# Performance work log

Hardware: AMD Instinct MI355X
Metric: run time of the kernel (lower is better)

Reference implementation:

```python
import jax, jax.numpy as jnp
import numpy as np

N_NODES = 10000
N_EDGES = 16384
D = 128            # node_in_dim == out_dim == edge_attr_dim == hidden_dim


def setup_inputs() -> dict:
    key = jax.random.key(0)
    ks = jax.random.split(key, 9)
    s = 1.0 / np.sqrt(D)
    x = jax.random.normal(ks[0], (N_NODES, D), dtype=jnp.float32)
    edge_index = jax.random.randint(ks[1], (2, N_EDGES), 0, N_NODES, dtype=jnp.int64)
    edge_attr = jax.random.normal(ks[2], (N_EDGES, D), dtype=jnp.float32)
    # edge_net: MLP 128 -> 128 (ReLU) -> 128*128
    w1 = jax.random.normal(ks[3], (D, D), dtype=jnp.float32) * s
    b1 = jnp.zeros((D,), dtype=jnp.float32)
    w2 = jax.random.normal(ks[4], (D, D * D), dtype=jnp.float32) * s
    b2 = jnp.zeros((D * D,), dtype=jnp.float32)
    # NNConv root weight and bias
    root = jax.random.normal(ks[5], (D, D), dtype=jnp.float32) * s
    bias = jnp.zeros((D,), dtype=jnp.float32)
    return {"x": x, "edge_index": edge_index, "edge_attr": edge_attr,
            "w1": w1, "b1": b1, "w2": w2, "b2": b2, "root": root, "bias": bias}


def reference(x, edge_index, edge_attr, w1, b1, w2, b2, root, bias):
    src, dst = edge_index[0], edge_index[1]
    # edge_net -> per-edge weight matrices [E, D, D]
    h = jax.nn.relu(edge_attr @ w1 + b1)
    w_edge = (h @ w2 + b2).reshape(-1, D, D)
    # gather source features, per-edge matvec: [E, D]
    x_j = x[src]
    msg = jnp.einsum('ei,eio->eo', x_j, w_edge)
    # scatter-mean into destination nodes
    seg_sum = jax.ops.segment_sum(msg, dst, num_segments=N_NODES)
    cnt = jax.ops.segment_sum(jnp.ones((msg.shape[0],), msg.dtype), dst,
                              num_segments=N_NODES)
    aggr = seg_sum / jnp.maximum(cnt, 1.0)[:, None]
    # NNConv root transform + bias
    conv_out = aggr + x @ root + bias
    # residual + exact GELU (torch nn.GELU default)
    return x + jax.nn.gelu(conv_out, approximate=False)
```

## Files before the change

### kernel.cpp

```cpp
#include <hip/hip_runtime.h>
#include <math.h>

#define D 128
#define NNODES 10000
#define NEDGES 16384
#define PADR 136
#define MAXDEG 16

typedef short short8 __attribute__((ext_vector_type(8)));
typedef float floatx4 __attribute__((ext_vector_type(4)));
typedef unsigned short ushortx4 __attribute__((ext_vector_type(4)));

__device__ __forceinline__ float bf2f(unsigned short u) {
  union { unsigned u; float f; } v; v.u = ((unsigned)u) << 16; return v.f;
}
__device__ __forceinline__ unsigned short f2bf(float f) {
  union { float f; unsigned u; } v; v.f = f;
  return (unsigned short)((v.u + 0x7FFFu + ((v.u >> 16) & 1u)) >> 16);
}
__device__ __forceinline__ float bflo(unsigned u) {
  union { unsigned u; float f; } v; v.u = u << 16; return v.f;
}
__device__ __forceinline__ float bfhi(unsigned u) {
  union { unsigned u; float f; } v; v.u = u & 0xFFFF0000u; return v.f;
}
__device__ __forceinline__ short8 pack8(float4 a, float4 b) {
  short8 r;
  r[0] = (short)f2bf(a.x); r[1] = (short)f2bf(a.y);
  r[2] = (short)f2bf(a.z); r[3] = (short)f2bf(a.w);
  r[4] = (short)f2bf(b.x); r[5] = (short)f2bf(b.y);
  r[6] = (short)f2bf(b.z); r[7] = (short)f2bf(b.w);
  return r;
}

__global__ __launch_bounds__(256) void k12(
    const float* __restrict__ x, const int* __restrict__ eidx,
    const float* __restrict__ ea,
    const float* __restrict__ w1, const float* __restrict__ b1,
    const float* __restrict__ w2, const float* __restrict__ b2,
    const float* __restrict__ root,
    unsigned short* __restrict__ w2t, unsigned short* __restrict__ rootT,
    unsigned short* __restrict__ hT, unsigned short* __restrict__ xjb,
    int* __restrict__ cnt) {
  __shared__ float L[32][129];
  __shared__ unsigned short w1tL[128 * PADR];
  const int t = threadIdx.x;
  const int bid = blockIdx.x;

  if (bid < 520) {
    if (bid < 40) { const int gid = bid * 256 + t; if (gid < NNODES) cnt[gid] = 0; }
    const float* __restrict__ src;
    unsigned short* dst;
    int o0;
    if (bid < 516) {
      const int k = bid >> 2;
      o0 = (bid & 3) * 32;
      src = (k < D) ? (w2 + (long)k * (D * D)) : b2;
      dst = w2t + (long)k * (D * PADR);
    } else {
      o0 = (bid - 516) * 32; src = root; dst = rootT;
    }
#pragma unroll
    for (int r = 0; r < 16; ++r) {
      int idx = r * 256 + t;
      int i = idx >> 5, oc = idx & 31;
      L[oc][i] = src[i * D + o0 + oc];
    }
    __syncthreads();
#pragma unroll
    for (int r = 0; r < 8; ++r) {
      int p = r * 256 + t;
      int oc = p >> 6, i2 = (p & 63) * 2;
      unsigned v = (unsigned)f2bf(L[oc][i2]) | ((unsigned)f2bf(L[oc][i2 + 1]) << 16);
      *(unsigned*)(dst + ((o0 + oc) * PADR + i2)) = v;
    }
    return;
  }

  const int e0 = (bid - 520) * 64;
#pragma unroll 4
  for (int r = 0; r < 16; ++r) {
    int idx = r * 256 + t, e = idx >> 6, i2 = (idx & 63) * 2;
    const int s = eidx[e0 + e];
    const float2 v = *(const float2*)(x + (long)s * D + i2);
    unsigned p = (unsigned)f2bf(v.x) | ((unsigned)f2bf(v.y) << 16);
    *(unsigned*)(xjb + ((e0 + e) * PADR + i2)) = p;
  }
  for (int c = 0; c < 4; ++c) {
    const int o0c = c * 32;
#pragma unroll
    for (int r = 0; r < 16; ++r) {
      int idx = r * 256 + t;
      int i = idx >> 5, oc = idx & 31;
      L[oc][i] = w1[i * D + o0c + oc];
    }
    __syncthreads();
#pragma unroll
    for (int r = 0; r < 8; ++r) {
      int p = r * 256 + t;
      int oc = p >> 6, i2 = (p & 63) * 2;
      unsigned v = (unsigned)f2bf(L[oc][i2]) | ((unsigned)f2bf(L[oc][i2 + 1]) << 16);
      *(unsigned*)(w1tL + ((o0c + oc) * PADR + i2)) = v;
    }
    __syncthreads();
  }
  const int lane = t & 63, w = t >> 6, lo = lane & 15, hi = lane >> 4;
  short8 af[4];
#pragma unroll
  for (int ks = 0; ks < 4; ++ks) {
    const float* p0 = ea + (long)(e0 + w * 16 + lo) * D + ks * 32 + hi * 8;
    af[ks] = pack8(*(const float4*)p0, *(const float4*)(p0 + 4));
  }
  floatx4 acc[8];
#pragma unroll
  for (int nt = 0; nt < 8; ++nt) acc[nt] = (floatx4){0.f, 0.f, 0.f, 0.f};
#pragma unroll
  for (int ks = 0; ks < 4; ++ks) {
    const int ib = ks * 32 + hi * 8;
#pragma unroll
    for (int nt = 0; nt < 8; ++nt) {
      const short8 bf_ = *(const short8*)&w1tL[(nt * 16 + lo) * PADR + ib];
      acc[nt] = __builtin_amdgcn_mfma_f32_16x16x32_bf16(af[ks], bf_, acc[nt], 0, 0, 0);
    }
  }
#pragma unroll
  for (int nt = 0; nt < 8; ++nt) {
    const int ko = nt * 16 + lo;
    const float b1v = b1[ko];
    float v0 = fmaxf(acc[nt][0] + b1v, 0.f);
    float v1 = fmaxf(acc[nt][1] + b1v, 0.f);
    float v2 = fmaxf(acc[nt][2] + b1v, 0.f);
    float v3 = fmaxf(acc[nt][3] + b1v, 0.f);
    uint2 pk;
    pk.x = (unsigned)f2bf(v0) | ((unsigned)f2bf(v1) << 16);
    pk.y = (unsigned)f2bf(v2) | ((unsigned)f2bf(v3) << 16);
    *(uint2*)(hT + (ko * NEDGES + e0 + w * 16 + hi * 4)) = pk;
  }
  if (t < 64) hT[128 * NEDGES + e0 + t] = 0x3F80;
}

__global__ __launch_bounds__(256, 3) void k3_msg(
    const unsigned short* __restrict__ w2t,
    const unsigned short* __restrict__ xjb,
    const unsigned short* __restrict__ hT,
    const int* __restrict__ eidx, int* __restrict__ cnt,
    int* __restrict__ elist,
    unsigned short* __restrict__ msgout) {
  __shared__ float hLT[65 * 128];
  const int t = threadIdx.x;
  const int b = blockIdx.x;
  const int kh = b & 1;
  const int oq = (b >> 1) & 3;
  const int eg = b >> 3;
  const int e0 = eg * 128;
  const int o0 = oq * 32;
  const int kbase = kh * 64;
  const int kcnt = kh ? 65 : 64;
  const int lane = t & 63, wv = t >> 6;
  const int lo = lane & 15, hi = lane >> 4;
  const int we = (wv >> 1) * 64;
  const int wo = (wv & 1) * 16;

  if ((b & 7) == 0 && t < 128) {
    const int e = e0 + t;
    const int d = eidx[NEDGES + e];
    const int pos = atomicAdd(&cnt[d], 1);
    if (pos < MAXDEG) elist[d * MAXDEG + pos] = e;
  }

  for (int idx = t; idx < kcnt * 64; idx += 256) {
    const int kk = idx >> 6, e2 = (idx & 63) * 2;
    const unsigned u = *(const unsigned*)&hT[(long)(kbase + kk) * NEDGES + e0 + e2];
    const int ebase = kk * 128;
#pragma unroll
    for (int q = 0; q < 2; ++q) {
      const int e = e2 + q;
      hLT[ebase + ((e >> 6) << 6) + ((e & 15) << 2) + ((e >> 4) & 3)] =
          q ? bfhi(u) : bflo(u);
    }
  }

  short8 xf[4][4];
#pragma unroll
  for (int ne = 0; ne < 4; ++ne)
#pragma unroll
    for (int ks = 0; ks < 4; ++ks)
      xf[ne][ks] = *(const short8*)&xjb[(long)(e0 + we + ne * 16 + lo) * PADR + ks * 32 + hi * 8];
  __syncthreads();

  const long kstride = (long)D * PADR;
  const unsigned short* ap = w2t + (long)kbase * kstride + (long)(o0 + wo + lo) * PADR + hi * 8;
  const float* hp = hLT + we + lo * 4;
  short8 a0[4], a1[4];
#pragma unroll
  for (int ks = 0; ks < 4; ++ks) a0[ks] = *(const short8*)(ap + ks * 32);
#pragma unroll
  for (int ks = 0; ks < 4; ++ks) a1[ks] = *(const short8*)(ap + kstride + ks * 32);
  floatx4 msg[4];
#pragma unroll
  for (int ne = 0; ne < 4; ++ne) msg[ne] = (floatx4){0.f, 0.f, 0.f, 0.f};

  auto body = [&](short8* fr, int k) {
    const floatx4 h4 = *(const floatx4*)(hp + k * 128);
    floatx4 P[4];
#pragma unroll
    for (int ne = 0; ne < 4; ++ne) P[ne] = (floatx4){0.f, 0.f, 0.f, 0.f};
#pragma unroll
    for (int ks = 0; ks < 4; ++ks)
#pragma unroll
      for (int ne = 0; ne < 4; ++ne)
        P[ne] = __builtin_amdgcn_mfma_f32_16x16x32_bf16(fr[ks], xf[ne][ks], P[ne], 0, 0, 0);
#pragma unroll
    for (int ne = 0; ne < 4; ++ne)
#pragma unroll
      for (int r = 0; r < 4; ++r) msg[ne][r] += h4[ne] * P[ne][r];
  };

  const int kpairs = kcnt >> 1;
  for (int j = 0; j < kpairs; ++j) {
    const int k = j * 2;
    body(a0, k);
    {
      const int kp = (k + 2 < kcnt) ? k + 2 : 0;
#pragma unroll
      for (int ks = 0; ks < 4; ++ks)
        a0[ks] = *(const short8*)(ap + (long)kp * kstride + ks * 32);
    }
    body(a1, k + 1);
    {
      const int kp = (k + 3 < kcnt) ? k + 3 : 0;
#pragma unroll
      for (int ks = 0; ks < 4; ++ks)
        a1[ks] = *(const short8*)(ap + (long)kp * kstride + ks * 32);
    }
  }
  if (kcnt & 1) body(a0, kcnt - 1);

#pragma unroll
  for (int ne = 0; ne < 4; ++ne) {
    const long e = e0 + we + ne * 16 + lo;
    uint2 pk;
    pk.x = (unsigned)f2bf(msg[ne][0]) | ((unsigned)f2bf(msg[ne][1]) << 16);
    pk.y = (unsigned)f2bf(msg[ne][2]) | ((unsigned)f2bf(msg[ne][3]) << 16);
    *(uint2*)(msgout + ((long)kh * NEDGES + e) * D + o0 + wo + hi * 4) = pk;
  }
}

__global__ __launch_bounds__(256) void k4_out(
    const float* __restrict__ x, const unsigned short* __restrict__ rootT,
    const float* __restrict__ bias, const unsigned short* __restrict__ msg,
    const int* __restrict__ cnt, const int* __restrict__ elist,
    float* __restrict__ out) {
  __shared__ float segL[64 * 132];
  const int t = threadIdx.x;
  const int n0 = blockIdx.x * 64;
  {
    const int ln = t >> 2;
    const int n = n0 + ln;
    const int oq = (t & 3) * 32;
    float a[32];
#pragma unroll
    for (int i = 0; i < 32; ++i) a[i] = 0.f;
    if (n < NNODES) {
      const int deg = min(cnt[n], MAXDEG);
      for (int j = 0; j < deg; ++j) {
        const int e = elist[n * MAXDEG + j];
        const unsigned short* r0 = msg + (long)e * D + oq;
        const unsigned short* r1 = r0 + (long)NEDGES * D;
#pragma unroll
        for (int q = 0; q < 4; ++q) {
          const uint4 u0 = *(const uint4*)(r0 + q * 8);
          const uint4 u1 = *(const uint4*)(r1 + q * 8);
          a[q * 8 + 0] += bflo(u0.x) + bflo(u1.x);
          a[q * 8 + 1] += bfhi(u0.x) + bfhi(u1.x);
          a[q * 8 + 2] += bflo(u0.y) + bflo(u1.y);
          a[q * 8 + 3] += bfhi(u0.y) + bfhi(u1.y);
          a[q * 8 + 4] += bflo(u0.z) + bflo(u1.z);
          a[q * 8 + 5] += bfhi(u0.z) + bfhi(u1.z);
          a[q * 8 + 6] += bflo(u0.w) + bflo(u1.w);
          a[q * 8 + 7] += bfhi(u0.w) + bfhi(u1.w);
        }
      }
    }
#pragma unroll
    for (int q = 0; q < 8; ++q)
      *(float4*)&segL[ln * 132 + oq + q * 4] =
          (float4){a[q * 4], a[q * 4 + 1], a[q * 4 + 2], a[q * 4 + 3]};
  }
  __syncthreads();
  const int lane = t & 63, w = t >> 6, lo = lane & 15, hi = lane >> 4;
  const int nrow = n0 + w * 16 + lo;
  short8 af[4];
#pragma unroll
  for (int ks = 0; ks < 4; ++ks) {
    if (nrow < NNODES) {
      const float* p0 = x + (long)nrow * D + ks * 32 + hi * 8;
      af[ks] = pack8(*(const float4*)p0, *(const float4*)(p0 + 4));
    } else {
      af[ks] = (short8){0, 0, 0, 0, 0, 0, 0, 0};
    }
  }
  floatx4 acc[8];
#pragma unroll
  for (int nt = 0; nt < 8; ++nt) acc[nt] = (floatx4){0.f, 0.f, 0.f, 0.f};
#pragma unroll
  for (int ks = 0; ks < 4; ++ks) {
    const int ib = ks * 32 + hi * 8;
#pragma unroll
    for (int nt = 0; nt < 8; ++nt) {
      const short8 bf_ = *(const short8*)&rootT[(nt * 16 + lo) * PADR + ib];
      acc[nt] = __builtin_amdgcn_mfma_f32_16x16x32_bf16(af[ks], bf_, acc[nt], 0, 0, 0);
    }
  }
  float dinv[4];
#pragma unroll
  for (int r = 0; r < 4; ++r) {
    const int n = n0 + w * 16 + hi * 4 + r;
    dinv[r] = (n < NNODES) ? 1.0f / fmaxf((float)cnt[n], 1.0f) : 0.f;
  }
#pragma unroll
  for (int nt = 0; nt < 8; ++nt) {
    const int co = nt * 16 + lo;
    const float bv = bias[co];
#pragma unroll
    for (int r = 0; r < 4; ++r) {
      const int n = n0 + w * 16 + hi * 4 + r;
      if (n < NNODES) {
        const float aggr = segL[(w * 16 + hi * 4 + r) * 132 + co] * dinv[r];
        const float v = acc[nt][r] + aggr + bv;
        const float ge = 0.5f * v * (1.0f + erff(v * 0.70710678f));
        out[(long)n * D + co] = x[(long)n * D + co] + ge;
      }
    }
  }
}

extern "C" void kernel_launch(void* const* d_in, const int* in_sizes, int n_in,
                              void* d_out, int out_size, void* d_ws, size_t ws_size,
                              hipStream_t stream) {
  (void)in_sizes; (void)n_in; (void)out_size; (void)ws_size;
  const float* x    = (const float*)d_in[0];
  const int*   eidx = (const int*)d_in[1];
  const float* ea   = (const float*)d_in[2];
  const float* w1   = (const float*)d_in[3];
  const float* b1   = (const float*)d_in[4];
  const float* w2   = (const float*)d_in[5];
  const float* b2   = (const float*)d_in[6];
  const float* root = (const float*)d_in[7];
  const float* bias = (const float*)d_in[8];
  float* out = (float*)d_out;
  char* ws = (char*)d_ws;
  unsigned short* hT    = (unsigned short*)(ws + 0);
  unsigned short* xjb   = (unsigned short*)(ws + 4227072);
  unsigned short* w2t   = (unsigned short*)(ws + 8683520);
  unsigned short* msg   = (unsigned short*)(ws + 13174784);
  int*            cnt   = (int*)(ws + 21563392);
  int*            elist = (int*)(ws + 21603392);
  unsigned short* rootT = (unsigned short*)(ws + 22243392);
  hipLaunchKernelGGL(k12, dim3(776), dim3(256), 0, stream,
                     x, eidx, ea, w1, b1, w2, b2, root, w2t, rootT, hT, xjb, cnt);
  hipLaunchKernelGGL(k3_msg, dim3(1024), dim3(256), 0, stream,
                     w2t, xjb, hT, eidx, cnt, elist, msg);
  hipLaunchKernelGGL(k4_out, dim3((NNODES + 63) / 64), dim3(256), 0, stream,
                     x, rootT, bias, msg, cnt, elist, out);
}
```

Before: 182.3 us.

## Switch message kernel to 32x32x16 MFMA with interleaved accumulator chains

Rewrites the per-edge message kernel so each wave computes a 32-output by 32-edge tile using 32x32x16 bf16 MFMA instead of 16x16x32. It alternates two accumulator chains so one chain's h-weighted reduction overlaps the other's MFMAs, and it prefetches the next k-plane's weights inside the MFMA loop. w2t is stored unpadded (stride D), hidden activations stay bf16 in shared memory (halving LDS), and the occupancy hint rises from 3 to 4 blocks. Risks include more register pressure from the 16-wide accumulators and possible LDS bank conflicts from the unpadded weight reads.

```diff
diff --git a/kernel.cpp b/kernel.cpp
--- a/kernel.cpp
+++ b/kernel.cpp
@@ -9,7 +9,7 @@
 
 typedef short short8 __attribute__((ext_vector_type(8)));
 typedef float floatx4 __attribute__((ext_vector_type(4)));
-typedef unsigned short ushortx4 __attribute__((ext_vector_type(4)));
+typedef float f32x16 __attribute__((ext_vector_type(16)));
 
 __device__ __forceinline__ float bf2f(unsigned short u) {
   union { unsigned u; float f; } v; v.u = ((unsigned)u) << 16; return v.f;
@@ -51,14 +51,15 @@
     if (bid < 40) { const int gid = bid * 256 + t; if (gid < NNODES) cnt[gid] = 0; }
     const float* __restrict__ src;
     unsigned short* dst;
-    int o0;
+    int o0, dstride;
     if (bid < 516) {
       const int k = bid >> 2;
       o0 = (bid & 3) * 32;
       src = (k < D) ? (w2 + (long)k * (D * D)) : b2;
-      dst = w2t + (long)k * (D * PADR);
+      dst = w2t + (long)k * (D * D);
+      dstride = D;
     } else {
-      o0 = (bid - 516) * 32; src = root; dst = rootT;
+      o0 = (bid - 516) * 32; src = root; dst = rootT; dstride = PADR;
     }
 #pragma unroll
     for (int r = 0; r < 16; ++r) {
@@ -72,7 +73,7 @@
       int p = r * 256 + t;
       int oc = p >> 6, i2 = (p & 63) * 2;
       unsigned v = (unsigned)f2bf(L[oc][i2]) | ((unsigned)f2bf(L[oc][i2 + 1]) << 16);
-      *(unsigned*)(dst + ((o0 + oc) * PADR + i2)) = v;
+      *(unsigned*)(dst + ((o0 + oc) * dstride + i2)) = v;
     }
     return;
   }
@@ -139,14 +140,14 @@
   if (t < 64) hT[128 * NEDGES + e0 + t] = 0x3F80;
 }
 
-__global__ __launch_bounds__(256, 3) void k3_msg(
+__global__ __launch_bounds__(256, 4) void k3_msg(
     const unsigned short* __restrict__ w2t,
     const unsigned short* __restrict__ xjb,
     const unsigned short* __restrict__ hT,
     const int* __restrict__ eidx, int* __restrict__ cnt,
     int* __restrict__ elist,
     unsigned short* __restrict__ msgout) {
-  __shared__ float hLT[65 * 128];
+  __shared__ unsigned short hLT[65 * 128];
   const int t = threadIdx.x;
   const int b = blockIdx.x;
   const int kh = b & 1;
@@ -157,9 +158,9 @@
   const int kbase = kh * 64;
   const int kcnt = kh ? 65 : 64;
   const int lane = t & 63, wv = t >> 6;
-  const int lo = lane & 15, hi = lane >> 4;
-  const int we = (wv >> 1) * 64;
-  const int wo = (wv & 1) * 16;
+  const int col = lane & 31;
+  const int hi = lane >> 5;
+  const int we = wv * 32;
 
   if ((b & 7) == 0 && t < 128) {
     const int e = e0 + t;
@@ -170,79 +171,72 @@
 
   for (int idx = t; idx < kcnt * 64; idx += 256) {
     const int kk = idx >> 6, e2 = (idx & 63) * 2;
-    const unsigned u = *(const unsigned*)&hT[(long)(kbase + kk) * NEDGES + e0 + e2];
-    const int ebase = kk * 128;
-#pragma unroll
-    for (int q = 0; q < 2; ++q) {
-      const int e = e2 + q;
-      hLT[ebase + ((e >> 6) << 6) + ((e & 15) << 2) + ((e >> 4) & 3)] =
-          q ? bfhi(u) : bflo(u);
-    }
-  }
-
-  short8 xf[4][4];
-#pragma unroll
-  for (int ne = 0; ne < 4; ++ne)
-#pragma unroll
-    for (int ks = 0; ks < 4; ++ks)
-      xf[ne][ks] = *(const short8*)&xjb[(long)(e0 + we + ne * 16 + lo) * PADR + ks * 32 + hi * 8];
+    *(unsigned*)&hLT[kk * 128 + e2] =
+        *(const unsigned*)&hT[(long)(kbase + kk) * NEDGES + e0 + e2];
+  }
+
+  short8 xf[8];
+  {
+    const unsigned short* xp = xjb + (long)(e0 + we + col) * PADR + hi * 8;
+#pragma unroll
+    for (int ks = 0; ks < 8; ++ks) xf[ks] = *(const short8*)(xp + ks * 16);
+  }
   __syncthreads();
 
-  const long kstride = (long)D * PADR;
-  const unsigned short* ap = w2t + (long)kbase * kstride + (long)(o0 + wo + lo) * PADR + hi * 8;
-  const float* hp = hLT + we + lo * 4;
-  short8 a0[4], a1[4];
-#pragma unroll
-  for (int ks = 0; ks < 4; ++ks) a0[ks] = *(const short8*)(ap + ks * 32);
-#pragma unroll
-  for (int ks = 0; ks < 4; ++ks) a1[ks] = *(const short8*)(ap + kstride + ks * 32);
-  floatx4 msg[4];
-#pragma unroll
-  for (int ne = 0; ne < 4; ++ne) msg[ne] = (floatx4){0.f, 0.f, 0.f, 0.f};
-
-  auto body = [&](short8* fr, int k) {
-    const floatx4 h4 = *(const floatx4*)(hp + k * 128);
-    floatx4 P[4];
-#pragma unroll
-    for (int ne = 0; ne < 4; ++ne) P[ne] = (floatx4){0.f, 0.f, 0.f, 0.f};
-#pragma unroll
-    for (int ks = 0; ks < 4; ++ks)
-#pragma unroll
-      for (int ne = 0; ne < 4; ++ne)
-        P[ne] = __builtin_amdgcn_mfma_f32_16x16x32_bf16(fr[ks], xf[ne][ks], P[ne], 0, 0, 0);
-#pragma unroll
-    for (int ne = 0; ne < 4; ++ne)
-#pragma unroll
-      for (int r = 0; r < 4; ++r) msg[ne][r] += h4[ne] * P[ne][r];
+  const long PLANE = (long)D * D;
+  const unsigned short* ap = w2t + (long)kbase * PLANE + (o0 + col) * D + hi * 8;
+  short8 a[8];
+#pragma unroll
+  for (int ks = 0; ks < 8; ++ks) a[ks] = *(const short8*)(ap + ks * 16);
+
+  f32x16 PA = (f32x16)0.f, PB = (f32x16)0.f, msg = (f32x16)0.f;
+  const unsigned short* hb = hLT + we + col;
+
+  auto chain = [&](f32x16& P, const unsigned short* nb) {
+#pragma unroll
+    for (int ks = 0; ks < 8; ++ks) {
+      P = __builtin_amdgcn_mfma_f32_32x32x16_bf16(a[ks], xf[ks], P, 0, 0, 0);
+      a[ks] = *(const short8*)(nb + ks * 16);
+    }
   };
-
-  const int kpairs = kcnt >> 1;
-  for (int j = 0; j < kpairs; ++j) {
-    const int k = j * 2;
-    body(a0, k);
-    {
-      const int kp = (k + 2 < kcnt) ? k + 2 : 0;
-#pragma unroll
-      for (int ks = 0; ks < 4; ++ks)
-        a0[ks] = *(const short8*)(ap + (long)kp * kstride + ks * 32);
-    }
-    body(a1, k + 1);
-    {
-      const int kp = (k + 3 < kcnt) ? k + 3 : 0;
-#pragma unroll
-      for (int ks = 0; ks < 4; ++ks)
-        a1[ks] = *(const short8*)(ap + (long)kp * kstride + ks * 32);
-    }
-  }
-  if (kcnt & 1) body(a0, kcnt - 1);
-
-#pragma unroll
-  for (int ne = 0; ne < 4; ++ne) {
-    const long e = e0 + we + ne * 16 + lo;
-    uint2 pk;
-    pk.x = (unsigned)f2bf(msg[ne][0]) | ((unsigned)f2bf(msg[ne][1]) << 16);
-    pk.y = (unsigned)f2bf(msg[ne][2]) | ((unsigned)f2bf(msg[ne][3]) << 16);
-    *(uint2*)(msgout + ((long)kh * NEDGES + e) * D + o0 + wo + hi * 4) = pk;
+  auto finish = [&](float h, const f32x16& P) {
+#pragma unroll
+    for (int r = 0; r < 16; ++r) msg[r] += h * P[r];
+  };
+
+  float hA = bf2f(hb[0]);
+  const unsigned short* nb = ap + PLANE;
+  chain(PA, nb);
+  int k = 1;
+  for (; k + 1 < kcnt; k += 2) {
+    nb += PLANE;
+    const float hBv = bf2f(hb[k * 128]);
+    chain(PB, nb);
+    finish(hA, PA); PA = (f32x16)0.f;
+    if (k + 2 < kcnt) nb += PLANE;
+    hA = bf2f(hb[(k + 1) * 128]);
+    chain(PA, nb);
+    finish(hBv, PB); PB = (f32x16)0.f;
+  }
+  if (k < kcnt) {
+    const float hBv = bf2f(hb[k * 128]);
+    chain(PB, nb);
+    finish(hA, PA);
+    finish(hBv, PB);
+  } else {
+    finish(hA, PA);
+  }
+
+  {
+    const long e = e0 + we + col;
+    unsigned short* mp = msgout + ((long)kh * NEDGES + e) * D + o0 + hi * 4;
+#pragma unroll
+    for (int g = 0; g < 4; ++g) {
+      uint2 pk;
+      pk.x = (unsigned)f2bf(msg[g * 4 + 0]) | ((unsigned)f2bf(msg[g * 4 + 1]) << 16);
+      pk.y = (unsigned)f2bf(msg[g * 4 + 2]) | ((unsigned)f2bf(msg[g * 4 + 3]) << 16);
+      *(uint2*)(mp + g * 8) = pk;
+    }
   }
 }
 
```

Measured after the change: 351.0 us. 92.6% more time.
